# Kernel optimization log

Measured on AMD Instinct MI355X. Metric: run time of the kernel, lower is better.

The kernel has to match this reference:

```python
import jax, jax.numpy as jnp
import numpy as np

N = 50000
E = 1600000
IN_DIM = 256
HID = 128
EPS = 1e-5


def _bn(x, gamma, beta):
    # BatchNorm1d forward in training mode: biased batch stats
    mean = jnp.mean(x, axis=0)
    var = jnp.mean((x - mean) ** 2, axis=0)
    return (x - mean) * jax.lax.rsqrt(var + EPS) * gamma + beta


def _sage(x, edge_index, Wl, bl, Wr):
    # PyG SAGEConv with mean aggregation:
    #   out = lin_l(mean_{j in N(i)} x_j) + lin_r(x_i)
    src, dst = edge_index[0], edge_index[1]
    agg = jax.ops.segment_sum(x[src], dst, num_segments=N)          # [N, H]
    cnt = jax.ops.segment_sum(jnp.ones((src.shape[0],), x.dtype), dst, num_segments=N)
    mean = agg / jnp.maximum(cnt, 1.0)[:, None]
    return mean @ Wl + bl + x @ Wr


def setup_inputs() -> dict:
    key = jax.random.key(0)
    ks = jax.random.split(key, 16)
    s_in = 1.0 / np.sqrt(IN_DIM)
    s_h = 1.0 / np.sqrt(HID)
    return {
        "x": jax.random.normal(ks[0], (N, IN_DIM), jnp.float32),
        "edge_index": jax.random.randint(ks[1], (2, E), 0, N, jnp.int32),
        # input_linear: Linear(IN_DIM, HID) + BN
        "W_in": jax.random.uniform(ks[2], (IN_DIM, HID), jnp.float32, -s_in, s_in),
        "b_in": jax.random.uniform(ks[3], (HID,), jnp.float32, -s_in, s_in),
        "g1": jnp.ones((HID,), jnp.float32), "be1": jnp.zeros((HID,), jnp.float32),
        # hidden_linear: Linear(HID, HID) + BN
        "W_hid": jax.random.uniform(ks[4], (HID, HID), jnp.float32, -s_h, s_h),
        "b_hid": jax.random.uniform(ks[5], (HID,), jnp.float32, -s_h, s_h),
        "g2": jnp.ones((HID,), jnp.float32), "be2": jnp.zeros((HID,), jnp.float32),
        # graph_conv1: SAGEConv(HID, HID) + BN
        "Wl1": jax.random.uniform(ks[6], (HID, HID), jnp.float32, -s_h, s_h),
        "bl1": jax.random.uniform(ks[7], (HID,), jnp.float32, -s_h, s_h),
        "Wr1": jax.random.uniform(ks[8], (HID, HID), jnp.float32, -s_h, s_h),
        "g3": jnp.ones((HID,), jnp.float32), "be3": jnp.zeros((HID,), jnp.float32),
        # graph_conv2: SAGEConv(HID, HID) + BN
        "Wl2": jax.random.uniform(ks[9], (HID, HID), jnp.float32, -s_h, s_h),
        "bl2": jax.random.uniform(ks[10], (HID,), jnp.float32, -s_h, s_h),
        "Wr2": jax.random.uniform(ks[11], (HID, HID), jnp.float32, -s_h, s_h),
        "g4": jnp.ones((HID,), jnp.float32), "be4": jnp.zeros((HID,), jnp.float32),
    }


def reference(x, edge_index, W_in, b_in, g1, be1, W_hid, b_hid, g2, be2,
              Wl1, bl1, Wr1, g3, be3, Wl2, bl2, Wr2, g4, be4):
    feat = jax.nn.relu(_bn(x @ W_in + b_in, g1, be1))
    feat = jax.nn.relu(_bn(feat @ W_hid + b_hid, g2, be2))
    out = _bn(_sage(feat, edge_index, Wl1, bl1, Wr1), g3, be3)
    out = _bn(_sage(out, edge_index, Wl2, bl2, Wr2), g4, be4)
    return (feat, out)
```

## Files before the change

kernel.cpp:

```cpp
#include <hip/hip_runtime.h>
#include <stdint.h>

#define NN 50000
#define EE 1600000
#define IN_DIMC 256
#define HIDC 128
#define EPSC 1e-5f

#define NB 196
#define GA 512
#define CHUNK 3125
#define STILE_SHIFT 13
#define NKEY 2048

typedef unsigned short ushort_t;
typedef __attribute__((ext_vector_type(8))) short short8;
typedef __attribute__((ext_vector_type(4))) float floatx4;

static __device__ inline ushort_t f2bf(float f) {
    unsigned int u = __float_as_uint(f);
    u = u + 0x7fffu + ((u >> 16) & 1u);
    return (ushort_t)(u >> 16);
}
static __device__ inline unsigned int pack2(float a, float b) {
    return (unsigned int)f2bf(a) | ((unsigned int)f2bf(b) << 16);
}
static __device__ inline float bf2f(unsigned int bits16) {
    return __uint_as_float(bits16 << 16);
}

__global__ __launch_bounds__(256) void tcvt_all_kernel(
    const float* __restrict__ W_in, const float* __restrict__ W_hid,
    const float* __restrict__ Wl1, const float* __restrict__ Wr1,
    const float* __restrict__ Wl2, const float* __restrict__ Wr2,
    ushort_t* __restrict__ Wt_in, ushort_t* __restrict__ Wt_hid,
    ushort_t* __restrict__ Wtl1, ushort_t* __restrict__ Wtr1,
    ushort_t* __restrict__ Wtl2, ushort_t* __restrict__ Wtr2)
{
    const int idx = blockIdx.x * 256 + threadIdx.x;
    if (idx < 32768) {
        const int n = idx >> 8;
        const int k = idx & 255;
        Wt_in[idx] = f2bf(W_in[(size_t)k * 128 + n]);
    } else if (idx < 32768 + 5 * 16384) {
        const int r = idx - 32768;
        const int seg = r / 16384;
        const int j = r - seg * 16384;
        const int n = j >> 7;
        const int k = j & 127;
        const float* W; ushort_t* Wt;
        switch (seg) {
            case 0: W = W_hid; Wt = Wt_hid; break;
            case 1: W = Wl1;  Wt = Wtl1;  break;
            case 2: W = Wr1;  Wt = Wtr1;  break;
            case 3: W = Wl2;  Wt = Wtl2;  break;
            default: W = Wr2; Wt = Wtr2;  break;
        }
        Wt[j] = f2bf(W[(size_t)k * 128 + n]);
    }
}

__global__ __launch_bounds__(512) void mfma_gemm_kernel(
    const void* __restrict__ A1, const ushort_t* __restrict__ Wt1, int K1, int a1type,
    const void* __restrict__ A2, const ushort_t* __restrict__ Wt2, int K2,
    const float* __restrict__ bias, float* __restrict__ Cf, ushort_t* __restrict__ Cb,
    int M, int affineSeg, int affineRelu,
    const float* __restrict__ preStats, const float* __restrict__ preG,
    const float* __restrict__ preBe, float* __restrict__ outStats)
{
    __shared__ ushort_t Bs[128 * 136];
    __shared__ __align__(16) float aArr[128], bArr[128];
    __shared__ float red_s[4][128], red_q[4][128];

    const int t    = threadIdx.x;
    const int lane = t & 63;
    const int wave = t >> 6;
    const int mt   = wave >> 1;
    const int nh   = wave & 1;
    const int quad = lane >> 4;
    const int l15  = lane & 15;
    const int row0 = blockIdx.x * 64;
    const int rowW = row0 + mt * 16;
    const int ksq  = quad * 8;

    if (affineSeg >= 0 && t < 128) {
        const float invM = 1.0f / (float)M;
        const float mean = preStats[t] * invM;
        float var = preStats[128 + t] * invM - mean * mean;
        if (var < 0.0f) var = 0.0f;
        const float s = preG[t] / sqrtf(var + EPSC);
        aArr[t] = s;
        bArr[t] = preBe[t] - mean * s;
    }

    floatx4 acc[4];
    #pragma unroll
    for (int j = 0; j < 4; j++)
        acc[j] = (floatx4){0.0f, 0.0f, 0.0f, 0.0f};

    int gr = rowW + l15;
    if (gr > M - 1) gr = M - 1;

    bool firstChunk = true;

    for (int s = 0; s < 2; s++) {
        const void*     A     = s ? A2  : A1;
        const ushort_t* Wt    = s ? Wt2 : Wt1;
        const int       K     = s ? K2  : K1;
        const int       atype = s ? 1   : a1type;
        const int       doAf  = (affineSeg == s);
        if (A == nullptr) continue;

        for (int kc = 0; kc < K; kc += 128) {
            if (!firstChunk) __syncthreads();
            firstChunk = false;

            #pragma unroll
            for (int p = 0; p < 4; p++) {
                const int idx = p * 512 + t;
                const int n   = idx >> 4;
                const int c0  = (idx & 15) * 8;
                *(uint4*)(Bs + n * 136 + c0) =
                    *(const uint4*)(Wt + (size_t)n * K + kc + c0);
            }
            __syncthreads();

            short8 afrag[4];
            if (atype == 1) {
                const ushort_t* Ab = (const ushort_t*)A;
                const size_t base = (size_t)gr * K + kc + ksq;
                #pragma unroll
                for (int ks = 0; ks < 4; ks++)
                    afrag[ks] = *(const short8*)(Ab + base + ks * 32);
                if (doAf) {
                    #pragma unroll
                    for (int ks = 0; ks < 4; ks++) {
                        const int k0 = kc + ks * 32 + ksq;
                        uint4 u = __builtin_bit_cast(uint4, afrag[ks]);
                        uint4 w;
                        unsigned int* up = (unsigned int*)&u;
                        unsigned int* wp = (unsigned int*)&w;
                        #pragma unroll
                        for (int h = 0; h < 4; h++) {
                            float lo = aArr[k0 + h * 2]     * bf2f(up[h] & 0xffffu) + bArr[k0 + h * 2];
                            float hi = aArr[k0 + h * 2 + 1] * bf2f(up[h] >> 16)     + bArr[k0 + h * 2 + 1];
                            if (affineRelu) { lo = fmaxf(lo, 0.0f); hi = fmaxf(hi, 0.0f); }
                            wp[h] = pack2(lo, hi);
                        }
                        afrag[ks] = __builtin_bit_cast(short8, w);
                    }
                }
            } else {
                const float* Af = (const float*)A;
                const size_t base = (size_t)gr * K + kc + ksq;
                #pragma unroll
                for (int ks = 0; ks < 4; ks++) {
                    float4 v0 = *(const float4*)(Af + base + ks * 32);
                    float4 v1 = *(const float4*)(Af + base + ks * 32 + 4);
                    if (doAf) {
                        const int k0 = kc + ks * 32 + ksq;
                        const float4 sa0 = *(const float4*)(aArr + k0);
                        const float4 sb0 = *(const float4*)(bArr + k0);
                        const float4 sa1 = *(const float4*)(aArr + k0 + 4);
                        const float4 sb1 = *(const float4*)(bArr + k0 + 4);
                        v0.x = sa0.x * v0.x + sb0.x;
                        v0.y = sa0.y * v0.y + sb0.y;
                        v0.z = sa0.z * v0.z + sb0.z;
                        v0.w = sa0.w * v0.w + sb0.w;
                        v1.x = sa1.x * v1.x + sb1.x;
                        v1.y = sa1.y * v1.y + sb1.y;
                        v1.z = sa1.z * v1.z + sb1.z;
                        v1.w = sa1.w * v1.w + sb1.w;
                        if (affineRelu) {
                            v0.x = fmaxf(v0.x, 0.0f); v0.y = fmaxf(v0.y, 0.0f);
                            v0.z = fmaxf(v0.z, 0.0f); v0.w = fmaxf(v0.w, 0.0f);
                            v1.x = fmaxf(v1.x, 0.0f); v1.y = fmaxf(v1.y, 0.0f);
                            v1.z = fmaxf(v1.z, 0.0f); v1.w = fmaxf(v1.w, 0.0f);
                        }
                    }
                    uint4 w;
                    w.x = pack2(v0.x, v0.y);
                    w.y = pack2(v0.z, v0.w);
                    w.z = pack2(v1.x, v1.y);
                    w.w = pack2(v1.z, v1.w);
                    afrag[ks] = __builtin_bit_cast(short8, w);
                }
            }

            #pragma unroll
            for (int ks = 0; ks < 4; ks++) {
                const int ko = ks * 32 + ksq;
                short8 b[4];
                #pragma unroll
                for (int j = 0; j < 4; j++)
                    b[j] = *(const short8*)(Bs + (nh * 64 + j * 16 + l15) * 136 + ko);
                #pragma unroll
                for (int j = 0; j < 4; j++)
                    acc[j] = __builtin_amdgcn_mfma_f32_16x16x32_bf16(
                        afrag[ks], b[j], acc[j], 0, 0, 0);
            }
        }
    }

    float s_[4], q_[4];
    #pragma unroll
    for (int j = 0; j < 4; j++) { s_[j] = 0.0f; q_[j] = 0.0f; }

    #pragma unroll
    for (int j = 0; j < 4; j++) {
        const int col = nh * 64 + j * 16 + l15;
        const float bv = bias[col];
        const int rbase = rowW + quad * 4;
        #pragma unroll
        for (int reg = 0; reg < 4; reg++) {
            const float val = acc[j][reg] + bv;
            const int r_ = rbase + reg;
            if (r_ < M) {
                if (Cf) Cf[(size_t)r_ * HIDC + col] = val;
                if (Cb) Cb[(size_t)r_ * HIDC + col] = f2bf(val);
                s_[j] += val;
                q_[j] += val * val;
            }
        }
    }
    #pragma unroll
    for (int j = 0; j < 4; j++) {
        s_[j] += __shfl_xor(s_[j], 16, 64);
        s_[j] += __shfl_xor(s_[j], 32, 64);
        q_[j] += __shfl_xor(q_[j], 16, 64);
        q_[j] += __shfl_xor(q_[j], 32, 64);
    }
    if (quad == 0) {
        #pragma unroll
        for (int j = 0; j < 4; j++) {
            red_s[mt][nh * 64 + j * 16 + l15] = s_[j];
            red_q[mt][nh * 64 + j * 16 + l15] = q_[j];
        }
    }
    __syncthreads();
    if (t < 128) {
        const float S = red_s[0][t] + red_s[1][t] + red_s[2][t] + red_s[3][t];
        const float Q = red_q[0][t] + red_q[1][t] + red_q[2][t] + red_q[3][t];
        atomicAdd(&outStats[t], S);
        atomicAdd(&outStats[128 + t], Q);
    }
}

__global__ __launch_bounds__(256) void bn_apply_kernel(
    const float* __restrict__ src, float* __restrict__ dstF,
    ushort_t* __restrict__ dstB, const float* __restrict__ stats,
    const float* __restrict__ gamma, const float* __restrict__ beta,
    int relu, int M)
{
    __shared__ float sc[128], sh[128];
    const int t = threadIdx.x;
    if (t < 128) {
        const float invM = 1.0f / (float)M;
        const float mean = stats[t] * invM;
        float var = stats[128 + t] * invM - mean * mean;
        if (var < 0.0f) var = 0.0f;
        const float s = gamma[t] / sqrtf(var + EPSC);
        sc[t] = s;
        sh[t] = beta[t] - mean * s;
    }
    __syncthreads();

    const int total4 = M * HIDC / 4;
    for (int i = blockIdx.x * 256 + t; i < total4; i += gridDim.x * 256) {
        float4 v = ((const float4*)src)[i];
        const int c = (i * 4) & 127;
        v.x = v.x * sc[c]     + sh[c];
        v.y = v.y * sc[c + 1] + sh[c + 1];
        v.z = v.z * sc[c + 2] + sh[c + 2];
        v.w = v.w * sc[c + 3] + sh[c + 3];
        if (relu) {
            v.x = fmaxf(v.x, 0.0f); v.y = fmaxf(v.y, 0.0f);
            v.z = fmaxf(v.z, 0.0f); v.w = fmaxf(v.w, 0.0f);
        }
        if (dstF) ((float4*)dstF)[i] = v;
        if (dstB) {
            uint2 w;
            w.x = pack2(v.x, v.y);
            w.y = pack2(v.z, v.w);
            *(uint2*)(dstB + (size_t)i * 4) = w;
        }
    }
}

__global__ __launch_bounds__(256) void bucket_hist_kernel(
    const int* __restrict__ dstArr, int* __restrict__ hist2D)
{
    __shared__ int hist[NB];
    const int t = threadIdx.x;
    for (int i = t; i < NB; i += 256) hist[i] = 0;
    __syncthreads();
    const int e0 = blockIdx.x * CHUNK;
    const int e1 = e0 + CHUNK;
    for (int e = e0 + t; e < e1; e += 256)
        atomicAdd(&hist[dstArr[e] >> 8], 1);
    __syncthreads();
    for (int i = t; i < NB; i += 256)
        hist2D[(size_t)i * GA + blockIdx.x] = hist[i];
}

__global__ __launch_bounds__(256) void bucket_offsets_kernel(
    int* __restrict__ hist2D, int* __restrict__ bucketBase, int* __restrict__ rowp)
{
    __shared__ int wtot[4];
    const int t = threadIdx.x;
    int tot = 0;
    if (t < NB) {
        int4* p = (int4*)(hist2D + (size_t)t * GA);
        int s = 0;
        for (int i = 0; i < GA / 4; i++) {
            int4 h = p[i];
            int4 o;
            o.x = s; s += h.x;
            o.y = s; s += h.y;
            o.z = s; s += h.z;
            o.w = s; s += h.w;
            p[i] = o;
        }
        tot = s;
    }
    const int lane = t & 63, w = t >> 6;
    int x = tot;
    #pragma unroll
    for (int off = 1; off < 64; off <<= 1) {
        const int y = __shfl_up(x, off);
        if (lane >= off) x += y;
    }
    if (lane == 63) wtot[w] = x;
    __syncthreads();
    int woff = 0;
    #pragma unroll
    for (int j = 0; j < 4; j++) if (j < w) woff += wtot[j];
    const int excl = x + woff - tot;
    if (t < NB) bucketBase[t] = excl;
    if (t == 0) { bucketBase[NB] = EE; rowp[NN] = EE; }
}

__global__ __launch_bounds__(256) void bucket_scatter_kernel(
    const int* __restrict__ srcArr, const int* __restrict__ dstArr,
    const int* __restrict__ hist2D, const int* __restrict__ bucketBase,
    unsigned int* __restrict__ ebuf)
{
    __shared__ int cur[NB];
    const int t = threadIdx.x;
    for (int i = t; i < NB; i += 256)
        cur[i] = bucketBase[i] + hist2D[(size_t)i * GA + blockIdx.x];
    __syncthreads();
    const int e0 = blockIdx.x * CHUNK;
    const int e1 = e0 + CHUNK;
    for (int e = e0 + t; e < e1; e += 256) {
        const int d = dstArr[e];
        const int s = srcArr[e];
        const int p = atomicAdd(&cur[d >> 8], 1);
        ebuf[p] = ((unsigned int)s << 16) | (unsigned int)d;
    }
}

__global__ __launch_bounds__(256) void fine_sort_kernel(
    const unsigned int* __restrict__ ebuf, const int* __restrict__ bucketBase,
    int* __restrict__ rowp, ushort_t* __restrict__ col)
{
    __shared__ int cnt[NKEY];
    __shared__ int wtot[4];
    const int b = blockIdx.x;
    const int t = threadIdx.x;
    const int bb0 = bucketBase[b];
    const int bb1 = bucketBase[b + 1];
    #pragma unroll
    for (int i = 0; i < 8; i++) cnt[t * 8 + i] = 0;
    __syncthreads();
    for (int e = bb0 + t; e < bb1; e += 256) {
        const unsigned int sd = ebuf[e];
        const int key = (int)((sd & 255u) << 3) | (int)(sd >> (16 + STILE_SHIFT));
        atomicAdd(&cnt[key], 1);
    }
    __syncthreads();
    int loc[8];
    int tot = 0;
    #pragma unroll
    for (int i = 0; i < 8; i++) { loc[i] = tot; tot += cnt[t * 8 + i]; }
    const int lane = t & 63, w = t >> 6;
    int x = tot;
    #pragma unroll
    for (int off = 1; off < 64; off <<= 1) {
        const int y = __shfl_up(x, off);
        if (lane >= off) x += y;
    }
    if (lane == 63) wtot[w] = x;
    __syncthreads();
    int woff = 0;
    #pragma unroll
    for (int j = 0; j < 4; j++) if (j < w) woff += wtot[j];
    const int excl = x + woff - tot;
    const int node = b * 256 + t;
    if (node < NN) rowp[node] = bb0 + excl;
    __syncthreads();
    #pragma unroll
    for (int i = 0; i < 8; i++) cnt[t * 8 + i] = excl + loc[i];
    __syncthreads();
    for (int e = bb0 + t; e < bb1; e += 256) {
        const unsigned int sd = ebuf[e];
        const int key = (int)((sd & 255u) << 3) | (int)(sd >> (16 + STILE_SHIFT));
        const int p = atomicAdd(&cnt[key], 1);
        col[bb0 + p] = (ushort_t)(sd >> 16);
    }
}

__global__ __launch_bounds__(256) void agg_kernel(
    const ushort_t* __restrict__ F, const int* __restrict__ row_ptr,
    const ushort_t* __restrict__ col, ushort_t* __restrict__ Mout,
    const float* __restrict__ preStats, const float* __restrict__ preG,
    const float* __restrict__ preBe)
{
    const int lane = threadIdx.x & 63;
    const int n = blockIdx.x * 4 + (threadIdx.x >> 6);
    const int coff = lane * 2;

    float sc0 = 1.0f, sh0 = 0.0f, sc1 = 1.0f, sh1 = 0.0f;
    if (preStats) {
        const float invM = 1.0f / (float)NN;
        const float m0 = preStats[coff] * invM;
        const float m1 = preStats[coff + 1] * invM;
        float v0 = preStats[128 + coff] * invM - m0 * m0;
        float v1 = preStats[128 + coff + 1] * invM - m1 * m1;
        if (v0 < 0.0f) v0 = 0.0f;
        if (v1 < 0.0f) v1 = 0.0f;
        sc0 = preG[coff] / sqrtf(v0 + EPSC);
        sc1 = preG[coff + 1] / sqrtf(v1 + EPSC);
        sh0 = preBe[coff] - m0 * sc0;
        sh1 = preBe[coff + 1] - m1 * sc1;
    }

    const int b = __builtin_amdgcn_readfirstlane(row_ptr[n]);
    const int e = __builtin_amdgcn_readfirstlane(row_ptr[n + 1]);
    const int deg = e - b;
    float accx = 0.0f, accy = 0.0f;
    int j = b;
    for (; j + 8 <= e; j += 8) {
        int s0[8];
        #pragma unroll
        for (int i = 0; i < 8; i++) s0[i] = col[j + i];
        unsigned int v0[8];
        #pragma unroll
        for (int i = 0; i < 8; i++)
            v0[i] = *(const unsigned int*)(F + (size_t)s0[i] * HIDC + coff);
        #pragma unroll
        for (int i = 0; i < 8; i++) {
            accx += bf2f(v0[i] & 0xffffu);
            accy += bf2f(v0[i] >> 16);
        }
    }
    for (; j < e; j++) {
        const unsigned int v = *(const unsigned int*)(F + (size_t)col[j] * HIDC + coff);
        accx += bf2f(v & 0xffffu);
        accy += bf2f(v >> 16);
    }
    float ox, oy;
    if (deg == 0) {
        ox = 0.0f; oy = 0.0f;
    } else {
        const float inv = 1.0f / (float)deg;
        ox = accx * inv * sc0 + (preStats ? sh0 : 0.0f);
        oy = accy * inv * sc1 + (preStats ? sh1 : 0.0f);
    }
    *(unsigned int*)(Mout + (size_t)n * HIDC + coff) = pack2(ox, oy);
}

extern "C" void kernel_launch(void* const* d_in, const int* in_sizes, int n_in,
                              void* d_out, int out_size, void* d_ws, size_t ws_size,
                              hipStream_t stream)
{
    const float* x     = (const float*)d_in[0];
    const int*   ei    = (const int*)  d_in[1];
    const float* W_in  = (const float*)d_in[2];
    const float* b_in  = (const float*)d_in[3];
    const float* g1    = (const float*)d_in[4];
    const float* be1   = (const float*)d_in[5];
    const float* W_hid = (const float*)d_in[6];
    const float* b_hid = (const float*)d_in[7];
    const float* g2    = (const float*)d_in[8];
    const float* be2   = (const float*)d_in[9];
    const float* Wl1   = (const float*)d_in[10];
    const float* bl1   = (const float*)d_in[11];
    const float* Wr1   = (const float*)d_in[12];
    const float* g3    = (const float*)d_in[13];
    const float* be3   = (const float*)d_in[14];
    const float* Wl2   = (const float*)d_in[15];
    const float* bl2   = (const float*)d_in[16];
    const float* Wr2   = (const float*)d_in[17];
    const float* g4    = (const float*)d_in[18];
    const float* be4   = (const float*)d_in[19];

    const int* srcArr = ei;
    const int* dstArr = ei + EE;

    char* ws = (char*)d_ws;
    float*    bufA      = (float*)ws;    ws += (size_t)NN * HIDC * sizeof(float);
    float*    bufB      = (float*)ws;    ws += (size_t)NN * HIDC * sizeof(float);
    ushort_t* featB16   = (ushort_t*)ws; ws += (size_t)NN * HIDC * sizeof(ushort_t);
    ushort_t* o3B16     = (ushort_t*)ws; ws += (size_t)NN * HIDC * sizeof(ushort_t);
    ushort_t* aggB16    = (ushort_t*)ws; ws += (size_t)NN * HIDC * sizeof(ushort_t);
    float*    stats     = (float*)ws;    ws += 4 * 256 * sizeof(float);
    int*      hist2D    = (int*)ws;      ws += (size_t)NB * GA * sizeof(int);
    int*      bucketBase= (int*)ws;      ws += (NB + 4) * sizeof(int);
    int*      rowp      = (int*)ws;      ws += (size_t)(NN + 4) * sizeof(int);
    ushort_t* colIdx    = (ushort_t*)ws; ws += (size_t)EE * sizeof(ushort_t) + 64;
    unsigned int* ebuf  = (unsigned int*)ws; ws += (size_t)EE * sizeof(unsigned int);
    ushort_t* Wt_in     = (ushort_t*)ws; ws += 128 * 256 * sizeof(ushort_t);
    ushort_t* Wt_hid    = (ushort_t*)ws; ws += 128 * 128 * sizeof(ushort_t);
    ushort_t* Wtl1      = (ushort_t*)ws; ws += 128 * 128 * sizeof(ushort_t);
    ushort_t* Wtr1      = (ushort_t*)ws; ws += 128 * 128 * sizeof(ushort_t);
    ushort_t* Wtl2      = (ushort_t*)ws; ws += 128 * 128 * sizeof(ushort_t);
    ushort_t* Wtr2      = (ushort_t*)ws; ws += 128 * 128 * sizeof(ushort_t);

    float* out0 = (float*)d_out;
    float* out1 = out0 + (size_t)NN * HIDC;

    hipMemsetAsync(stats, 0, 4 * 256 * sizeof(float), stream);

    tcvt_all_kernel<<<448, 256, 0, stream>>>(W_in, W_hid, Wl1, Wr1, Wl2, Wr2,
                                             Wt_in, Wt_hid, Wtl1, Wtr1, Wtl2, Wtr2);

    bucket_hist_kernel<<<GA, 256, 0, stream>>>(dstArr, hist2D);
    bucket_offsets_kernel<<<1, 256, 0, stream>>>(hist2D, bucketBase, rowp);
    bucket_scatter_kernel<<<GA, 256, 0, stream>>>(srcArr, dstArr, hist2D,
                                                  bucketBase, ebuf);
    fine_sort_kernel<<<NB, 256, 0, stream>>>(ebuf, bucketBase, rowp, colIdx);

    const int gemmGrid = (NN + 63) / 64;

    mfma_gemm_kernel<<<gemmGrid, 512, 0, stream>>>(
        x, Wt_in, IN_DIMC, 0, nullptr, nullptr, 0,
        b_in, bufA, nullptr, NN, -1, 0, nullptr, nullptr, nullptr, stats + 0);

    mfma_gemm_kernel<<<gemmGrid, 512, 0, stream>>>(
        bufA, Wt_hid, HIDC, 0, nullptr, nullptr, 0,
        b_hid, bufB, nullptr, NN, 0, 1, stats + 0, g1, be1, stats + 256);

    bn_apply_kernel<<<1024, 256, 0, stream>>>(bufB, out0, featB16,
                                              stats + 256, g2, be2, 1, NN);

    agg_kernel<<<12500, 256, 0, stream>>>(featB16, rowp, colIdx, aggB16,
                                          nullptr, nullptr, nullptr);
    mfma_gemm_kernel<<<gemmGrid, 512, 0, stream>>>(
        aggB16, Wtl1, HIDC, 1, featB16, Wtr1, HIDC,
        bl1, nullptr, o3B16, NN, -1, 0, nullptr, nullptr, nullptr, stats + 512);

    agg_kernel<<<12500, 256, 0, stream>>>(o3B16, rowp, colIdx, aggB16,
                                          stats + 512, g3, be3);
    mfma_gemm_kernel<<<gemmGrid, 512, 0, stream>>>(
        aggB16, Wtl2, HIDC, 1, o3B16, Wtr2, HIDC,
        bl2, bufB, nullptr, NN, 1, 0, stats + 512, g3, be3, stats + 768);

    bn_apply_kernel<<<1024, 256, 0, stream>>>(bufB, out1, nullptr,
                                              stats + 768, g4, be4, 0, NN);
}
```

Baseline: 469.3 us.

## Spread BN stat atomics over slots, parallelize bucket scan, persistent agg waves

BN statistic accumulation now spreads its atomics across 8 slot copies indexed by block, and consumers sum the slots, to cut contention on 256 addresses. The single-block serial scan over the bucket histogram is split into a per-bucket parallel scan kernel plus a small base-offset kernel. The aggregation kernel becomes grid-stride with 4096 blocks instead of one wave per node. These add an extra launch and some redundant slot reads in every consumer.

```diff
diff --git a/kernel.cpp b/kernel.cpp
--- a/kernel.cpp
+++ b/kernel.cpp
@@ -12,6 +12,9 @@
 #define CHUNK 3125
 #define STILE_SHIFT 13
 #define NKEY 2048
+
+#define NSLOT 8
+#define STATS_STRIDE (NSLOT * 256)
 
 typedef unsigned short ushort_t;
 typedef __attribute__((ext_vector_type(8))) short short8;
@@ -84,9 +87,15 @@
     const int ksq  = quad * 8;
 
     if (affineSeg >= 0 && t < 128) {
+        float sS = 0.0f, sQ = 0.0f;
+        #pragma unroll
+        for (int s8 = 0; s8 < NSLOT; s8++) {
+            sS += preStats[s8 * 256 + t];
+            sQ += preStats[s8 * 256 + 128 + t];
+        }
         const float invM = 1.0f / (float)M;
-        const float mean = preStats[t] * invM;
-        float var = preStats[128 + t] * invM - mean * mean;
+        const float mean = sS * invM;
+        float var = sQ * invM - mean * mean;
         if (var < 0.0f) var = 0.0f;
         const float s = preG[t] / sqrtf(var + EPSC);
         aArr[t] = s;
@@ -241,8 +250,9 @@
     if (t < 128) {
         const float S = red_s[0][t] + red_s[1][t] + red_s[2][t] + red_s[3][t];
         const float Q = red_q[0][t] + red_q[1][t] + red_q[2][t] + red_q[3][t];
-        atomicAdd(&outStats[t], S);
-        atomicAdd(&outStats[128 + t], Q);
+        float* slot = outStats + (blockIdx.x & (NSLOT - 1)) * 256;
+        atomicAdd(&slot[t], S);
+        atomicAdd(&slot[128 + t], Q);
     }
 }
 
@@ -255,9 +265,15 @@
     __shared__ float sc[128], sh[128];
     const int t = threadIdx.x;
     if (t < 128) {
+        float sS = 0.0f, sQ = 0.0f;
+        #pragma unroll
+        for (int s8 = 0; s8 < NSLOT; s8++) {
+            sS += stats[s8 * 256 + t];
+            sQ += stats[s8 * 256 + 128 + t];
+        }
         const float invM = 1.0f / (float)M;
-        const float mean = stats[t] * invM;
-        float var = stats[128 + t] * invM - mean * mean;
+        const float mean = sS * invM;
+        float var = sQ * invM - mean * mean;
         if (var < 0.0f) var = 0.0f;
         const float s = gamma[t] / sqrtf(var + EPSC);
         sc[t] = s;
@@ -303,26 +319,41 @@
         hist2D[(size_t)i * GA + blockIdx.x] = hist[i];
 }
 
-__global__ __launch_bounds__(256) void bucket_offsets_kernel(
-    int* __restrict__ hist2D, int* __restrict__ bucketBase, int* __restrict__ rowp)
+__global__ __launch_bounds__(256) void bucket_scan_kernel(
+    int* __restrict__ hist2D, int* __restrict__ rowTot)
+{
+    __shared__ int wtot[4];
+    const int b = blockIdx.x;
+    const int t = threadIdx.x;
+    int* row = hist2D + (size_t)b * GA;
+    const int v0 = row[2 * t];
+    const int v1 = row[2 * t + 1];
+    const int pair = v0 + v1;
+    const int lane = t & 63, w = t >> 6;
+    int x = pair;
+    #pragma unroll
+    for (int off = 1; off < 64; off <<= 1) {
+        const int y = __shfl_up(x, off);
+        if (lane >= off) x += y;
+    }
+    if (lane == 63) wtot[w] = x;
+    __syncthreads();
+    int woff = 0;
+    #pragma unroll
+    for (int j = 0; j < 4; j++) if (j < w) woff += wtot[j];
+    const int excl = x + woff - pair;
+    row[2 * t]     = excl;
+    row[2 * t + 1] = excl + v0;
+    if (t == 255) rowTot[b] = excl + pair;
+}
+
+__global__ __launch_bounds__(256) void bucket_base_kernel(
+    const int* __restrict__ rowTot, int* __restrict__ bucketBase,
+    int* __restrict__ rowp)
 {
     __shared__ int wtot[4];
     const int t = threadIdx.x;
-    int tot = 0;
-    if (t < NB) {
-        int4* p = (int4*)(hist2D + (size_t)t * GA);
-        int s = 0;
-        for (int i = 0; i < GA / 4; i++) {
-            int4 h = p[i];
-            int4 o;
-            o.x = s; s += h.x;
-            o.y = s; s += h.y;
-            o.z = s; s += h.z;
-            o.w = s; s += h.w;
-            p[i] = o;
-        }
-        tot = s;
-    }
+    const int tot = (t < NB) ? rowTot[t] : 0;
     const int lane = t & 63, w = t >> 6;
     int x = tot;
     #pragma unroll
@@ -417,16 +448,26 @@
     const float* __restrict__ preBe)
 {
     const int lane = threadIdx.x & 63;
-    const int n = blockIdx.x * 4 + (threadIdx.x >> 6);
+    const int wave = blockIdx.x * 4 + (threadIdx.x >> 6);
+    const int nwaves = gridDim.x * 4;
     const int coff = lane * 2;
 
     float sc0 = 1.0f, sh0 = 0.0f, sc1 = 1.0f, sh1 = 0.0f;
-    if (preStats) {
+    const int doAf = (preStats != nullptr);
+    if (doAf) {
+        float s0 = 0.0f, s1 = 0.0f, q0 = 0.0f, q1 = 0.0f;
+        #pragma unroll
+        for (int s8 = 0; s8 < NSLOT; s8++) {
+            s0 += preStats[s8 * 256 + coff];
+            s1 += preStats[s8 * 256 + coff + 1];
+            q0 += preStats[s8 * 256 + 128 + coff];
+            q1 += preStats[s8 * 256 + 128 + coff + 1];
+        }
         const float invM = 1.0f / (float)NN;
-        const float m0 = preStats[coff] * invM;
-        const float m1 = preStats[coff + 1] * invM;
-        float v0 = preStats[128 + coff] * invM - m0 * m0;
-        float v1 = preStats[128 + coff + 1] * invM - m1 * m1;
+        const float m0 = s0 * invM;
+        const float m1 = s1 * invM;
+        float v0 = q0 * invM - m0 * m0;
+        float v1 = q1 * invM - m1 * m1;
         if (v0 < 0.0f) v0 = 0.0f;
         if (v1 < 0.0f) v1 = 0.0f;
         sc0 = preG[coff] / sqrtf(v0 + EPSC);
@@ -435,39 +476,42 @@
         sh1 = preBe[coff + 1] - m1 * sc1;
     }
 
-    const int b = __builtin_amdgcn_readfirstlane(row_ptr[n]);
-    const int e = __builtin_amdgcn_readfirstlane(row_ptr[n + 1]);
-    const int deg = e - b;
-    float accx = 0.0f, accy = 0.0f;
-    int j = b;
-    for (; j + 8 <= e; j += 8) {
-        int s0[8];
-        #pragma unroll
-        for (int i = 0; i < 8; i++) s0[i] = col[j + i];
-        unsigned int v0[8];
-        #pragma unroll
-        for (int i = 0; i < 8; i++)
-            v0[i] = *(const unsigned int*)(F + (size_t)s0[i] * HIDC + coff);
-        #pragma unroll
-        for (int i = 0; i < 8; i++) {
-            accx += bf2f(v0[i] & 0xffffu);
-            accy += bf2f(v0[i] >> 16);
-        }
-    }
-    for (; j < e; j++) {
-        const unsigned int v = *(const unsigned int*)(F + (size_t)col[j] * HIDC + coff);
-        accx += bf2f(v & 0xffffu);
-        accy += bf2f(v >> 16);
-    }
-    float ox, oy;
-    if (deg == 0) {
-        ox = 0.0f; oy = 0.0f;
-    } else {
-        const float inv = 1.0f / (float)deg;
-        ox = accx * inv * sc0 + (preStats ? sh0 : 0.0f);
-        oy = accy * inv * sc1 + (preStats ? sh1 : 0.0f);
-    }
-    *(unsigned int*)(Mout + (size_t)n * HIDC + coff) = pack2(ox, oy);
+    for (int n = wave; n < NN; n += nwaves) {
+        const int b = __builtin_amdgcn_readfirstlane(row_ptr[n]);
+        const int e = __builtin_amdgcn_readfirstlane(row_ptr[n + 1]);
+        const int deg = e - b;
+        float accx = 0.0f, accy = 0.0f;
+        int j = b;
+        for (; j + 8 <= e; j += 8) {
+            int s0[8];
+            #pragma unroll
+            for (int i = 0; i < 8; i++) s0[i] = col[j + i];
+            unsigned int v0[8];
+            #pragma unroll
+            for (int i = 0; i < 8; i++)
+                v0[i] = *(const unsigned int*)(F + (size_t)s0[i] * HIDC + coff);
+            #pragma unroll
+            for (int i = 0; i < 8; i++) {
+                accx += bf2f(v0[i] & 0xffffu);
+                accy += bf2f(v0[i] >> 16);
+            }
+        }
+        for (; j < e; j++) {
+            const unsigned int v = *(const unsigned int*)(F + (size_t)col[j] * HIDC + coff);
+            accx += bf2f(v & 0xffffu);
+            accy += bf2f(v >> 16);
+        }
+        float ox, oy;
+        if (deg == 0) {
+            ox = 0.0f; oy = 0.0f;
+        } else {
+            const float inv = 1.0f / (float)deg;
+            ox = accx * inv;
+            oy = accy * inv;
+            if (doAf) { ox = ox * sc0 + sh0; oy = oy * sc1 + sh1; }
+        }
+        *(unsigned int*)(Mout + (size_t)n * HIDC + coff) = pack2(ox, oy);
+    }
 }
 
 extern "C" void kernel_launch(void* const* d_in, const int* in_sizes, int n_in,
@@ -504,8 +548,9 @@
     ushort_t* featB16   = (ushort_t*)ws; ws += (size_t)NN * HIDC * sizeof(ushort_t);
     ushort_t* o3B16     = (ushort_t*)ws; ws += (size_t)NN * HIDC * sizeof(ushort_t);
     ushort_t* aggB16    = (ushort_t*)ws; ws += (size_t)NN * HIDC * sizeof(ushort_t);
-    float*    stats     = (float*)ws;    ws += 4 * 256 * sizeof(float);
+    float*    stats     = (float*)ws;    ws += 4 * STATS_STRIDE * sizeof(float);
     int*      hist2D    = (int*)ws;      ws += (size_t)NB * GA * sizeof(int);
+    int*      rowTot    = (int*)ws;      ws += (NB + 4) * sizeof(int);
     int*      bucketBase= (int*)ws;      ws += (NB + 4) * sizeof(int);
     int*      rowp      = (int*)ws;      ws += (size_t)(NN + 4) * sizeof(int);
     ushort_t* colIdx    = (ushort_t*)ws; ws += (size_t)EE * sizeof(ushort_t) + 64;
@@ -520,13 +565,14 @@
     float* out0 = (float*)d_out;
     float* out1 = out0 + (size_t)NN * HIDC;
 
-    hipMemsetAsync(stats, 0, 4 * 256 * sizeof(float), stream);
+    hipMemsetAsync(stats, 0, 4 * STATS_STRIDE * sizeof(float), stream);
 
     tcvt_all_kernel<<<448, 256, 0, stream>>>(W_in, W_hid, Wl1, Wr1, Wl2, Wr2,
                                              Wt_in, Wt_hid, Wtl1, Wtr1, Wtl2, Wtr2);
 
     bucket_hist_kernel<<<GA, 256, 0, stream>>>(dstArr, hist2D);
-    bucket_offsets_kernel<<<1, 256, 0, stream>>>(hist2D, bucketBase, rowp);
+    bucket_scan_kernel<<<NB, 256, 0, stream>>>(hist2D, rowTot);
+    bucket_base_kernel<<<1, 256, 0, stream>>>(rowTot, bucketBase, rowp);
     bucket_scatter_kernel<<<GA, 256, 0, stream>>>(srcArr, dstArr, hist2D,
                                                   bucketBase, ebuf);
     fine_sort_kernel<<<NB, 256, 0, stream>>>(ebuf, bucketBase, rowp, colIdx);
@@ -535,27 +581,31 @@
 
     mfma_gemm_kernel<<<gemmGrid, 512, 0, stream>>>(
         x, Wt_in, IN_DIMC, 0, nullptr, nullptr, 0,
-        b_in, bufA, nullptr, NN, -1, 0, nullptr, nullptr, nullptr, stats + 0);
+        b_in, bufA, nullptr, NN, -1, 0, nullptr, nullptr, nullptr,
+        stats + 0 * STATS_STRIDE);
 
     mfma_gemm_kernel<<<gemmGrid, 512, 0, stream>>>(
         bufA, Wt_hid, HIDC, 0, nullptr, nullptr, 0,
-        b_hid, bufB, nullptr, NN, 0, 1, stats + 0, g1, be1, stats + 256);
+        b_hid, bufB, nullptr, NN, 0, 1, stats + 0 * STATS_STRIDE, g1, be1,
+        stats + 1 * STATS_STRIDE);
 
     bn_apply_kernel<<<1024, 256, 0, stream>>>(bufB, out0, featB16,
-                                              stats + 256, g2, be2, 1, NN);
-
-    agg_kernel<<<12500, 256, 0, stream>>>(featB16, rowp, colIdx, aggB16,
-                                          nullptr, nullptr, nullptr);
+                                              stats + 1 * STATS_STRIDE, g2, be2, 1, NN);
+
+    agg_kernel<<<4096, 256, 0, stream>>>(featB16, rowp, colIdx, aggB16,
+                                         nullptr, nullptr, nullptr);
     mfma_gemm_kernel<<<gemmGrid, 512, 0, stream>>>(
         aggB16, Wtl1, HIDC, 1, featB16, Wtr1, HIDC,
-        bl1, nullptr, o3B16, NN, -1, 0, nullptr, nullptr, nullptr, stats + 512);
-
-    agg_kernel<<<12500, 256, 0, stream>>>(o3B16, rowp, colIdx, aggB16,
-                                          stats + 512, g3, be3);
+        bl1, nullptr, o3B16, NN, -1, 0, nullptr, nullptr, nullptr,
+        stats + 2 * STATS_STRIDE);
+
+    agg_kernel<<<4096, 256, 0, stream>>>(o3B16, rowp, colIdx, aggB16,
+                                         stats + 2 * STATS_STRIDE, g3, be3);
     mfma_gemm_kernel<<<gemmGrid, 512, 0, stream>>>(
         aggB16, Wtl2, HIDC, 1, o3B16, Wtr2, HIDC,
-        bl2, bufB, nullptr, NN, 1, 0, stats + 512, g3, be3, stats + 768);
+        bl2, bufB, nullptr, NN, 1, 0, stats + 2 * STATS_STRIDE, g3, be3,
+        stats + 3 * STATS_STRIDE);
 
     bn_apply_kernel<<<1024, 256, 0, stream>>>(bufB, out1, nullptr,
-                                              stats + 768, g4, be4, 0, NN);
-}
+                                              stats + 3 * STATS_STRIDE, g4, be4, 0, NN);
+}
```

After: 400.9 us. -14.6%, faster.
